# Kernel tuning notes

Measured on AMD Instinct MI355X. Metric: run time of the kernel, lower is better.

The kernel has to match this reference:

```python
import jax, jax.numpy as jnp
import numpy as np

B, C, H, W = 64, 256, 64, 64
RATIO, K = 16, 8
PLANES = C // 2          # context_modeling hidden = int(in_planes*0.5)
HIDDEN = C // RATIO      # net hidden
ATT_CH = K // 2          # kernel-attention hidden
TEMP = 30.0
EPS = 1e-5


def setup_inputs() -> dict:
    key = jax.random.key(0)
    ks = jax.random.split(key, 16)
    s = lambda k, shape: jax.random.normal(k, shape, dtype=jnp.float32) * 0.05
    return {
        "x": jax.random.normal(ks[0], (B, C, H, W), dtype=jnp.float32),
        # conv_mask: Conv2d(C,1,1) with bias
        "w_mask": s(ks[1], (1, C)), "b_mask": jnp.zeros((1,), jnp.float32),
        # context_modeling: Conv2d(C,PLANES,1)+bias, LayerNorm([PLANES,1,1]), GELU, Conv2d(PLANES,C,1)+bias
        "w_cm1": s(ks[2], (PLANES, C)), "b_cm1": jnp.zeros((PLANES,), jnp.float32),
        "ln_w": jnp.ones((PLANES,), jnp.float32), "ln_b": jnp.zeros((PLANES,), jnp.float32),
        "w_cm2": s(ks[3], (C, PLANES)), "b_cm2": jnp.zeros((C,), jnp.float32),
        # net: Conv2d(C,HIDDEN,1,bias=False), ReLU, Conv2d(HIDDEN,K,1,bias=False)
        "w_net1": s(ks[4], (HIDDEN, C)), "w_net2": s(ks[5], (K, HIDDEN)),
        # kernel attention branch (K != 1)
        "w_fc": s(ks[6], (ATT_CH, K)),
        "bn_w": jnp.ones((ATT_CH,), jnp.float32), "bn_b": jnp.zeros((ATT_CH,), jnp.float32),
        "bn_mean": jnp.zeros((ATT_CH,), jnp.float32), "bn_var": jnp.ones((ATT_CH,), jnp.float32),
        "w_kfc": s(ks[7], (K, ATT_CH)),
    }


def reference(x, w_mask, b_mask, w_cm1, b_cm1, ln_w, ln_b, w_cm2, b_cm2,
              w_net1, w_net2, w_fc, bn_w, bn_b, bn_mean, bn_var, w_kfc):
    b, c, h, w = x.shape
    # beta_c: global average pool -> [B, C]
    beta_c = jnp.mean(x, axis=(2, 3))
    # global_pool: softmax(conv_mask(x)) over HW, spatially weighted sum of x
    mask = jnp.einsum('bchw,oc->bohw', x, w_mask)[:, 0] + b_mask[0]      # [B,H,W]
    mask = jax.nn.softmax(mask.reshape(b, h * w), axis=-1)               # softmax over HW
    context = jnp.einsum('bchw,bs->bc', x, mask.reshape(b, h, w).reshape(b, -1).reshape(b, h * w)) if False else \
        jnp.einsum('bcs,bs->bc', x.reshape(b, c, h * w), mask)           # [B,C]
    # context_modeling: 1x1 conv -> LayerNorm over channels -> GELU -> 1x1 conv
    t = context @ w_cm1.T + b_cm1                                        # [B, PLANES]
    mu = jnp.mean(t, axis=-1, keepdims=True)
    var = jnp.mean((t - mu) ** 2, axis=-1, keepdims=True)
    t = (t - mu) * jax.lax.rsqrt(var + EPS) * ln_w + ln_b
    t = jax.nn.gelu(t, approximate=False)
    beta_g = t @ w_cm2.T + b_cm2                                         # [B, C]
    # beta_s: channel-mean/max maps, tiled [avg,max,avg,max,...], spatial mean
    a = jnp.mean(jnp.mean(x, axis=1), axis=(1, 2))                       # [B]
    m = jnp.mean(jnp.max(x, axis=1), axis=(1, 2))                        # [B]
    beta_s = jnp.tile(jnp.stack([a, m], axis=-1), (1, c // 2))           # [B, C]
    out = beta_c + beta_g + beta_s                                       # [B, C]
    # net: conv1x1 -> ReLU -> conv1x1
    out = jax.nn.relu(out @ w_net1.T) @ w_net2.T                         # [B, K]
    # dynamic kernel attention (eval-mode BatchNorm on 1x1 spatial)
    ka = out @ w_fc.T                                                    # [B, K/2]
    ka = (ka - bn_mean) * jax.lax.rsqrt(bn_var + EPS) * bn_w + bn_b
    kernel = jax.nn.sigmoid(jax.nn.relu(ka) @ w_kfc.T)                   # [B, K]
    out = out * kernel
    return jax.nn.softmax(out / TEMP, axis=-1)                           # [B, K]
```

## Files before the change

kernel.cpp:

```cpp
#include <hip/hip_runtime.h>
#include <math.h>

#define BB   64
#define CC   256
#define HWQ  4096
#define TILE 64
#define TPB  256

#define WS_BETA 0
#define WS_CTX  16384
#define WS_Z    32768
#define WS_M    32832
#define WS_N    32896

__global__ void zero_ws(float* __restrict__ ws, int n) {
    int i = blockIdx.x * blockDim.x + threadIdx.x;
    if (i < n) ws[i] = 0.0f;
}

__global__ __launch_bounds__(TPB) void pass1(
    const float* __restrict__ x,
    const float* __restrict__ w_mask,
    const float* __restrict__ b_mask,
    float* __restrict__ ws)
{
    __shared__ __align__(16) float tileX[CC * TILE];
    __shared__ __align__(16) float wm[CC];
    __shared__ __align__(16) float redL[16 * 16 * 4];
    __shared__ __align__(16) float redM[16 * 16 * 4];
    __shared__ __align__(16) float tileP[TILE];

    float* beta_sum = ws + WS_BETA;
    float* ctx_sum  = ws + WS_CTX;
    float* Zsum     = ws + WS_Z;
    float* msum     = ws + WS_M;

    const int tid = threadIdx.x;
    const int b   = blockIdx.x >> 6;
    const int t0  = (blockIdx.x & 63) * TILE;

    wm[tid] = w_mask[tid];
    __syncthreads();

    const int hi = tid >> 4;
    const int j  = tid & 15;
    const float* xb = x + (size_t)b * CC * HWQ;

    float lp0 = 0.f, lp1 = 0.f, lp2 = 0.f, lp3 = 0.f;
    float mp0 = -3.4e38f, mp1 = -3.4e38f, mp2 = -3.4e38f, mp3 = -3.4e38f;

    #pragma unroll
    for (int i = 0; i < 16; ++i) {
        const int c = i * 16 + hi;
        const float4 v = *reinterpret_cast<const float4*>(xb + (size_t)c * HWQ + t0 + 4 * j);
        *reinterpret_cast<float4*>(&tileX[c * TILE + 4 * j]) = v;
        const float w = wm[c];
        lp0 = fmaf(w, v.x, lp0); lp1 = fmaf(w, v.y, lp1);
        lp2 = fmaf(w, v.z, lp2); lp3 = fmaf(w, v.w, lp3);
        mp0 = fmaxf(mp0, v.x); mp1 = fmaxf(mp1, v.y);
        mp2 = fmaxf(mp2, v.z); mp3 = fmaxf(mp3, v.w);
    }
    reinterpret_cast<float4*>(redL)[tid] = make_float4(lp0, lp1, lp2, lp3);
    reinterpret_cast<float4*>(redM)[tid] = make_float4(mp0, mp1, mp2, mp3);
    __syncthreads();

    if (tid < TILE) {
        float lg = 0.f, cm = -3.4e38f;
        #pragma unroll
        for (int h = 0; h < 16; ++h) {
            lg += redL[h * 64 + tid];
            cm = fmaxf(cm, redM[h * 64 + tid]);
        }
        lg += b_mask[0];
        const float p = expf(lg);
        tileP[tid] = p;
        float zs = p, cs = cm;
        #pragma unroll
        for (int off = 32; off > 0; off >>= 1) {
            zs += __shfl_down(zs, off, 64);
            cs += __shfl_down(cs, off, 64);
        }
        if (tid == 0) {
            atomicAdd(&Zsum[b], zs);
            atomicAdd(&msum[b], cs);
        }
    }
    __syncthreads();

    {
        const int c = tid;
        const float4* xr = reinterpret_cast<const float4*>(&tileX[c * TILE]);
        const float4* pr = reinterpret_cast<const float4*>(tileP);
        float sm = 0.f, cx = 0.f;
        #pragma unroll
        for (int s4 = 0; s4 < 16; ++s4) {
            const int idx = (s4 + c) & 15;
            const float4 xv = xr[idx];
            const float4 pv = pr[idx];
            sm += xv.x + xv.y + xv.z + xv.w;
            cx = fmaf(xv.x, pv.x, cx); cx = fmaf(xv.y, pv.y, cx);
            cx = fmaf(xv.z, pv.z, cx); cx = fmaf(xv.w, pv.w, cx);
        }
        atomicAdd(&beta_sum[b * CC + c], sm);
        atomicAdd(&ctx_sum[b * CC + c], cx);
    }
}

__global__ __launch_bounds__(TPB) void finalize(
    const float* __restrict__ ws,
    const float* __restrict__ w_cm1,  const float* __restrict__ b_cm1,
    const float* __restrict__ ln_w,   const float* __restrict__ ln_b,
    const float* __restrict__ w_cm2,  const float* __restrict__ b_cm2,
    const float* __restrict__ w_net1, const float* __restrict__ w_net2,
    const float* __restrict__ w_fc,   const float* __restrict__ bn_w,
    const float* __restrict__ bn_b,   const float* __restrict__ bn_mean,
    const float* __restrict__ bn_var, const float* __restrict__ w_kfc,
    float* __restrict__ out)
{
    __shared__ __align__(16) float s_beta[CC];
    __shared__ __align__(16) float s_ctx[CC];
    __shared__ __align__(16) float s_t[128];
    __shared__ __align__(16) float s_out[CC];
    __shared__ float s_h[16];
    __shared__ float s_o2[8];
    __shared__ float s_red[4];
    __shared__ float s_scal[4];

    const float* beta_sum = ws + WS_BETA;
    const float* ctx_sum  = ws + WS_CTX;
    const float* Zsum     = ws + WS_Z;
    const float* msum     = ws + WS_M;

    const int b = blockIdx.x, tid = threadIdx.x;

    const float bc = beta_sum[b * CC + tid] * (1.f / 4096.f);
    const float cx = ctx_sum[b * CC + tid] / Zsum[b];
    s_beta[tid] = bc;
    s_ctx[tid]  = cx;

    float av = bc;
    #pragma unroll
    for (int off = 32; off > 0; off >>= 1) av += __shfl_down(av, off, 64);
    if ((tid & 63) == 0) s_red[tid >> 6] = av;
    __syncthreads();
    if (tid == 0) {
        s_scal[0] = (s_red[0] + s_red[1] + s_red[2] + s_red[3]) * (1.f / 256.f);
        s_scal[1] = msum[b] * (1.f / 4096.f);
    }
    __syncthreads();

    if (tid < 128) {
        const float4* wr = reinterpret_cast<const float4*>(w_cm1 + tid * 256);
        const float4* cr = reinterpret_cast<const float4*>(s_ctx);
        float acc = 0.f;
        #pragma unroll 4
        for (int i = 0; i < 64; ++i) {
            const float4 w = wr[i], c4 = cr[i];
            acc = fmaf(w.x, c4.x, acc); acc = fmaf(w.y, c4.y, acc);
            acc = fmaf(w.z, c4.z, acc); acc = fmaf(w.w, c4.w, acc);
        }
        s_t[tid] = acc + b_cm1[tid];
    }
    __syncthreads();

    if (tid < 64) {
        float v = s_t[tid] + s_t[tid + 64];
        #pragma unroll
        for (int off = 32; off > 0; off >>= 1) v += __shfl_down(v, off, 64);
        float mu = __shfl(v, 0, 64) * (1.f / 128.f);
        const float d0 = s_t[tid] - mu, d1 = s_t[tid + 64] - mu;
        float vv = d0 * d0 + d1 * d1;
        #pragma unroll
        for (int off = 32; off > 0; off >>= 1) vv += __shfl_down(vv, off, 64);
        if (tid == 0) {
            s_scal[2] = mu;
            s_scal[3] = rsqrtf(vv * (1.f / 128.f) + 1e-5f);
        }
    }
    __syncthreads();

    if (tid < 128) {
        float g = (s_t[tid] - s_scal[2]) * s_scal[3] * ln_w[tid] + ln_b[tid];
        g = 0.5f * g * (1.0f + erff(g * 0.70710678118654752f));
        s_t[tid] = g;
    }
    __syncthreads();

    {
        const float4* wr = reinterpret_cast<const float4*>(w_cm2 + tid * 128);
        const float4* gr = reinterpret_cast<const float4*>(s_t);
        float acc = 0.f;
        #pragma unroll 4
        for (int i = 0; i < 32; ++i) {
            const float4 w = wr[i], g = gr[i];
            acc = fmaf(w.x, g.x, acc); acc = fmaf(w.y, g.y, acc);
            acc = fmaf(w.z, g.z, acc); acc = fmaf(w.w, g.w, acc);
        }
        const float bs = (tid & 1) ? s_scal[1] : s_scal[0];
        s_out[tid] = s_beta[tid] + acc + b_cm2[tid] + bs;
    }
    __syncthreads();

    if (tid < 16) {
        const float4* wr = reinterpret_cast<const float4*>(w_net1 + tid * 256);
        const float4* orr = reinterpret_cast<const float4*>(s_out);
        float acc = 0.f;
        #pragma unroll 4
        for (int i = 0; i < 64; ++i) {
            const float4 w = wr[i], o = orr[i];
            acc = fmaf(w.x, o.x, acc); acc = fmaf(w.y, o.y, acc);
            acc = fmaf(w.z, o.z, acc); acc = fmaf(w.w, o.w, acc);
        }
        s_h[tid] = fmaxf(acc, 0.f);
    }
    __syncthreads();

    if (tid < 8) {
        float acc = 0.f;
        #pragma unroll
        for (int jj = 0; jj < 16; ++jj) acc += s_h[jj] * w_net2[tid * 16 + jj];
        s_o2[tid] = acc;
    }
    __syncthreads();

    if (tid == 0) {
        float r[4];
        #pragma unroll
        for (int q = 0; q < 4; ++q) {
            float acc = 0.f;
            #pragma unroll
            for (int k = 0; k < 8; ++k) acc += s_o2[k] * w_fc[q * 8 + k];
            acc = (acc - bn_mean[q]) * rsqrtf(bn_var[q] + 1e-5f) * bn_w[q] + bn_b[q];
            r[q] = fmaxf(acc, 0.f);
        }
        float v[8], vmax = -3.4e38f;
        #pragma unroll
        for (int k = 0; k < 8; ++k) {
            float acc = 0.f;
            #pragma unroll
            for (int q = 0; q < 4; ++q) acc += r[q] * w_kfc[k * 4 + q];
            const float kr = 1.f / (1.f + expf(-acc));
            v[k] = s_o2[k] * kr * (1.f / 30.f);
            vmax = fmaxf(vmax, v[k]);
        }
        float zs = 0.f;
        #pragma unroll
        for (int k = 0; k < 8; ++k) { v[k] = expf(v[k] - vmax); zs += v[k]; }
        const float inv = 1.f / zs;
        #pragma unroll
        for (int k = 0; k < 8; ++k) out[b * 8 + k] = v[k] * inv;
    }
}

extern "C" void kernel_launch(void* const* d_in, const int* in_sizes, int n_in,
                              void* d_out, int out_size, void* d_ws, size_t ws_size,
                              hipStream_t stream) {
    const float* x       = (const float*)d_in[0];
    const float* w_mask  = (const float*)d_in[1];
    const float* b_mask  = (const float*)d_in[2];
    const float* w_cm1   = (const float*)d_in[3];
    const float* b_cm1   = (const float*)d_in[4];
    const float* ln_w    = (const float*)d_in[5];
    const float* ln_b    = (const float*)d_in[6];
    const float* w_cm2   = (const float*)d_in[7];
    const float* b_cm2   = (const float*)d_in[8];
    const float* w_net1  = (const float*)d_in[9];
    const float* w_net2  = (const float*)d_in[10];
    const float* w_fc    = (const float*)d_in[11];
    const float* bn_w    = (const float*)d_in[12];
    const float* bn_b    = (const float*)d_in[13];
    const float* bn_mean = (const float*)d_in[14];
    const float* bn_var  = (const float*)d_in[15];
    const float* w_kfc   = (const float*)d_in[16];
    float* out = (float*)d_out;
    float* ws  = (float*)d_ws;

    zero_ws<<<(WS_N + 255) / 256, 256, 0, stream>>>(ws, WS_N);
    pass1<<<BB * (HWQ / TILE), TPB, 0, stream>>>(x, w_mask, b_mask, ws);
    finalize<<<BB, TPB, 0, stream>>>(ws, w_cm1, b_cm1, ln_w, ln_b, w_cm2, b_cm2,
                                     w_net1, w_net2, w_fc, bn_w, bn_b, bn_mean,
                                     bn_var, w_kfc, out);
}
```

Measured before the change: 410.5 us.

## Loop each block over eight tiles with register prefetch; write per-block partials instead of atomics

The first pass now launches 8 blocks per batch instead of 64. Each block loops over 8 spatial tiles, double-buffering the next tile's x values in registers while it reduces the current one, and keeps its channel sums in registers rather than staging the tile in shared memory. Per-block partial sums for beta, context, Z and the max-mean go to distinct workspace slots, and the finalize kernel adds them up. This removes the global atomics and the zeroing kernel. The cost is lower block-level parallelism and higher register pressure from the two 16-float4 buffers, which may cut occupancy and the number of memory requests in flight.

```diff
diff --git a/kernel.cpp b/kernel.cpp
--- a/kernel.cpp
+++ b/kernel.cpp
@@ -5,104 +5,133 @@
 #define CC   256
 #define HWQ  4096
 #define TILE 64
+#define ITER 8
+#define QB   8
+#define NBLK (BB * QB)
 #define TPB  256
 
 #define WS_BETA 0
-#define WS_CTX  16384
-#define WS_Z    32768
-#define WS_M    32832
-#define WS_N    32896
-
-__global__ void zero_ws(float* __restrict__ ws, int n) {
-    int i = blockIdx.x * blockDim.x + threadIdx.x;
-    if (i < n) ws[i] = 0.0f;
-}
-
-__global__ __launch_bounds__(TPB) void pass1(
+#define WS_CTX  (NBLK * CC)
+#define WS_Z    (2 * NBLK * CC)
+#define WS_M    (WS_Z + NBLK)
+
+__global__ __launch_bounds__(TPB, 2) void pass1(
     const float* __restrict__ x,
     const float* __restrict__ w_mask,
     const float* __restrict__ b_mask,
     float* __restrict__ ws)
 {
-    __shared__ __align__(16) float tileX[CC * TILE];
     __shared__ __align__(16) float wm[CC];
-    __shared__ __align__(16) float redL[16 * 16 * 4];
-    __shared__ __align__(16) float redM[16 * 16 * 4];
+    __shared__ __align__(16) float redL[1024];
+    __shared__ __align__(16) float redM[1024];
     __shared__ __align__(16) float tileP[TILE];
-
-    float* beta_sum = ws + WS_BETA;
-    float* ctx_sum  = ws + WS_CTX;
-    float* Zsum     = ws + WS_Z;
-    float* msum     = ws + WS_M;
+    __shared__ __align__(16) float scrA[CC * 16];
+    __shared__ __align__(16) float scrB[CC * 16];
 
     const int tid = threadIdx.x;
-    const int b   = blockIdx.x >> 6;
-    const int t0  = (blockIdx.x & 63) * TILE;
+    const int b   = blockIdx.x >> 3;
+    const int q   = blockIdx.x & 7;
+    const int hi  = tid >> 4;
+    const int j   = tid & 15;
+    const float* xb = x + (size_t)b * CC * HWQ + q * (TILE * ITER);
 
     wm[tid] = w_mask[tid];
-    __syncthreads();
-
-    const int hi = tid >> 4;
-    const int j  = tid & 15;
-    const float* xb = x + (size_t)b * CC * HWQ;
-
-    float lp0 = 0.f, lp1 = 0.f, lp2 = 0.f, lp3 = 0.f;
-    float mp0 = -3.4e38f, mp1 = -3.4e38f, mp2 = -3.4e38f, mp3 = -3.4e38f;
-
+
+    float4 cur[16], nxt[16];
     #pragma unroll
     for (int i = 0; i < 16; ++i) {
         const int c = i * 16 + hi;
-        const float4 v = *reinterpret_cast<const float4*>(xb + (size_t)c * HWQ + t0 + 4 * j);
-        *reinterpret_cast<float4*>(&tileX[c * TILE + 4 * j]) = v;
-        const float w = wm[c];
-        lp0 = fmaf(w, v.x, lp0); lp1 = fmaf(w, v.y, lp1);
-        lp2 = fmaf(w, v.z, lp2); lp3 = fmaf(w, v.w, lp3);
-        mp0 = fmaxf(mp0, v.x); mp1 = fmaxf(mp1, v.y);
-        mp2 = fmaxf(mp2, v.z); mp3 = fmaxf(mp3, v.w);
-    }
-    reinterpret_cast<float4*>(redL)[tid] = make_float4(lp0, lp1, lp2, lp3);
-    reinterpret_cast<float4*>(redM)[tid] = make_float4(mp0, mp1, mp2, mp3);
-    __syncthreads();
-
-    if (tid < TILE) {
-        float lg = 0.f, cm = -3.4e38f;
-        #pragma unroll
-        for (int h = 0; h < 16; ++h) {
-            lg += redL[h * 64 + tid];
-            cm = fmaxf(cm, redM[h * 64 + tid]);
-        }
-        lg += b_mask[0];
-        const float p = expf(lg);
-        tileP[tid] = p;
-        float zs = p, cs = cm;
-        #pragma unroll
-        for (int off = 32; off > 0; off >>= 1) {
-            zs += __shfl_down(zs, off, 64);
-            cs += __shfl_down(cs, off, 64);
-        }
-        if (tid == 0) {
-            atomicAdd(&Zsum[b], zs);
-            atomicAdd(&msum[b], cs);
-        }
-    }
-    __syncthreads();
-
+        cur[i] = *reinterpret_cast<const float4*>(xb + (size_t)c * HWQ + 4 * j);
+    }
+    __syncthreads();
+    const float bm = b_mask[0];
+
+    float smP[16], cxP[16];
+    #pragma unroll
+    for (int i = 0; i < 16; ++i) { smP[i] = 0.f; cxP[i] = 0.f; }
+    float zTot = 0.f, mTot = 0.f;
+
+    for (int it = 0; it < ITER; ++it) {
+        float lp0 = 0.f, lp1 = 0.f, lp2 = 0.f, lp3 = 0.f;
+        float mp0 = -3.4e38f, mp1 = -3.4e38f, mp2 = -3.4e38f, mp3 = -3.4e38f;
+        #pragma unroll
+        for (int i = 0; i < 16; ++i) {
+            const float w = wm[i * 16 + hi];
+            const float4 v = cur[i];
+            lp0 = fmaf(w, v.x, lp0); lp1 = fmaf(w, v.y, lp1);
+            lp2 = fmaf(w, v.z, lp2); lp3 = fmaf(w, v.w, lp3);
+            mp0 = fmaxf(mp0, v.x); mp1 = fmaxf(mp1, v.y);
+            mp2 = fmaxf(mp2, v.z); mp3 = fmaxf(mp3, v.w);
+        }
+        reinterpret_cast<float4*>(redL)[tid] = make_float4(lp0, lp1, lp2, lp3);
+        reinterpret_cast<float4*>(redM)[tid] = make_float4(mp0, mp1, mp2, mp3);
+        __syncthreads();
+
+        if (tid < TILE) {
+            float lg = 0.f, cm = -3.4e38f;
+            #pragma unroll
+            for (int h = 0; h < 16; ++h) {
+                lg += redL[h * 64 + tid];
+                cm = fmaxf(cm, redM[h * 64 + tid]);
+            }
+            const float p = expf(lg + bm);
+            tileP[tid] = p;
+            float zs = p, cs = cm;
+            #pragma unroll
+            for (int off = 32; off > 0; off >>= 1) {
+                zs += __shfl_down(zs, off, 64);
+                cs += __shfl_down(cs, off, 64);
+            }
+            if (tid == 0) { zTot += zs; mTot += cs; }
+        }
+        __syncthreads();
+
+        if (it + 1 < ITER) {
+            #pragma unroll
+            for (int i = 0; i < 16; ++i) {
+                const int c = i * 16 + hi;
+                nxt[i] = *reinterpret_cast<const float4*>(
+                    xb + (size_t)c * HWQ + (it + 1) * TILE + 4 * j);
+            }
+        }
+
+        const float4 pv = reinterpret_cast<const float4*>(tileP)[j];
+        #pragma unroll
+        for (int i = 0; i < 16; ++i) {
+            const float4 v = cur[i];
+            smP[i] += (v.x + v.y) + (v.z + v.w);
+            cxP[i] = fmaf(v.x, pv.x, fmaf(v.y, pv.y,
+                     fmaf(v.z, pv.z, fmaf(v.w, pv.w, cxP[i]))));
+        }
+        if (it + 1 < ITER) {
+            #pragma unroll
+            for (int i = 0; i < 16; ++i) cur[i] = nxt[i];
+        }
+    }
+
+    #pragma unroll
+    for (int i = 0; i < 16; ++i) {
+        scrA[(i * 16 + hi) * 16 + j] = smP[i];
+        scrB[(i * 16 + hi) * 16 + j] = cxP[i];
+    }
+    __syncthreads();
     {
         const int c = tid;
-        const float4* xr = reinterpret_cast<const float4*>(&tileX[c * TILE]);
-        const float4* pr = reinterpret_cast<const float4*>(tileP);
+        const float4* a4 = reinterpret_cast<const float4*>(&scrA[c * 16]);
+        const float4* b4 = reinterpret_cast<const float4*>(&scrB[c * 16]);
         float sm = 0.f, cx = 0.f;
         #pragma unroll
-        for (int s4 = 0; s4 < 16; ++s4) {
-            const int idx = (s4 + c) & 15;
-            const float4 xv = xr[idx];
-            const float4 pv = pr[idx];
-            sm += xv.x + xv.y + xv.z + xv.w;
-            cx = fmaf(xv.x, pv.x, cx); cx = fmaf(xv.y, pv.y, cx);
-            cx = fmaf(xv.z, pv.z, cx); cx = fmaf(xv.w, pv.w, cx);
-        }
-        atomicAdd(&beta_sum[b * CC + c], sm);
-        atomicAdd(&ctx_sum[b * CC + c], cx);
+        for (int g = 0; g < 4; ++g) {
+            const float4 av = a4[g], bv = b4[g];
+            sm += (av.x + av.y) + (av.z + av.w);
+            cx += (bv.x + bv.y) + (bv.z + bv.w);
+        }
+        ws[WS_BETA + blockIdx.x * CC + c] = sm;
+        ws[WS_CTX  + blockIdx.x * CC + c] = cx;
+    }
+    if (tid == 0) {
+        ws[WS_Z + blockIdx.x] = zTot;
+        ws[WS_M + blockIdx.x] = mTot;
     }
 }
 
@@ -125,16 +154,28 @@
     __shared__ float s_o2[8];
     __shared__ float s_red[4];
     __shared__ float s_scal[4];
-
-    const float* beta_sum = ws + WS_BETA;
-    const float* ctx_sum  = ws + WS_CTX;
-    const float* Zsum     = ws + WS_Z;
-    const float* msum     = ws + WS_M;
+    __shared__ float s_zm[2];
 
     const int b = blockIdx.x, tid = threadIdx.x;
 
-    const float bc = beta_sum[b * CC + tid] * (1.f / 4096.f);
-    const float cx = ctx_sum[b * CC + tid] / Zsum[b];
+    float bc_s = 0.f, cx_s = 0.f;
+    #pragma unroll
+    for (int qq = 0; qq < QB; ++qq) {
+        bc_s += ws[WS_BETA + (b * QB + qq) * CC + tid];
+        cx_s += ws[WS_CTX  + (b * QB + qq) * CC + tid];
+    }
+    if (tid < 16) {
+        float v = (tid < 8) ? ws[WS_Z + b * QB + tid] : ws[WS_M + b * QB + (tid - 8)];
+        v += __shfl_down(v, 4, 64);
+        v += __shfl_down(v, 2, 64);
+        v += __shfl_down(v, 1, 64);
+        if (tid == 0) s_zm[0] = v;
+        if (tid == 8) s_zm[1] = v;
+    }
+    __syncthreads();
+
+    const float bc = bc_s * (1.f / 4096.f);
+    const float cx = cx_s / s_zm[0];
     s_beta[tid] = bc;
     s_ctx[tid]  = cx;
 
@@ -145,7 +186,7 @@
     __syncthreads();
     if (tid == 0) {
         s_scal[0] = (s_red[0] + s_red[1] + s_red[2] + s_red[3]) * (1.f / 256.f);
-        s_scal[1] = msum[b] * (1.f / 4096.f);
+        s_scal[1] = s_zm[1] * (1.f / 4096.f);
     }
     __syncthreads();
 
@@ -226,19 +267,19 @@
     if (tid == 0) {
         float r[4];
         #pragma unroll
-        for (int q = 0; q < 4; ++q) {
+        for (int p = 0; p < 4; ++p) {
             float acc = 0.f;
             #pragma unroll
-            for (int k = 0; k < 8; ++k) acc += s_o2[k] * w_fc[q * 8 + k];
-            acc = (acc - bn_mean[q]) * rsqrtf(bn_var[q] + 1e-5f) * bn_w[q] + bn_b[q];
-            r[q] = fmaxf(acc, 0.f);
+            for (int k = 0; k < 8; ++k) acc += s_o2[k] * w_fc[p * 8 + k];
+            acc = (acc - bn_mean[p]) * rsqrtf(bn_var[p] + 1e-5f) * bn_w[p] + bn_b[p];
+            r[p] = fmaxf(acc, 0.f);
         }
         float v[8], vmax = -3.4e38f;
         #pragma unroll
         for (int k = 0; k < 8; ++k) {
             float acc = 0.f;
             #pragma unroll
-            for (int q = 0; q < 4; ++q) acc += r[q] * w_kfc[k * 4 + q];
+            for (int p = 0; p < 4; ++p) acc += r[p] * w_kfc[k * 4 + p];
             const float kr = 1.f / (1.f + expf(-acc));
             v[k] = s_o2[k] * kr * (1.f / 30.f);
             vmax = fmaxf(vmax, v[k]);
@@ -275,8 +316,7 @@
     float* out = (float*)d_out;
     float* ws  = (float*)d_ws;
 
-    zero_ws<<<(WS_N + 255) / 256, 256, 0, stream>>>(ws, WS_N);
-    pass1<<<BB * (HWQ / TILE), TPB, 0, stream>>>(x, w_mask, b_mask, ws);
+    pass1<<<NBLK, TPB, 0, stream>>>(x, w_mask, b_mask, ws);
     finalize<<<BB, TPB, 0, stream>>>(ws, w_cm1, b_cm1, ln_w, ln_b, w_cm2, b_cm2,
                                      w_net1, w_net2, w_fc, bn_w, bn_b, bn_mean,
                                      bn_var, w_kfc, out);
```

After: 410.8 us. Within noise of the previous version (+0.1%).
